# Performance work log

Measured on AMD Instinct MI355X. Metric: run time of the kernel, lower is better.

## Reference

```python
import jax, jax.numpy as jnp
import numpy as np

# Faithful distillation of AttentionNet's cross-modal attention block.
# The resnet50/PointNet backbones are replaced by their output feature maps
# (img: [B,256,64,64], pc2d: [B,2048,64,64]) supplied as inputs, since the
# kernel-relevant math is the conv1x1 projections + bmm/softmax/bmm attention,
# followed by global avg-pool, concat, and the fc + log_softmax head.
# Note: the original forward contains a bug (img_v1 overwritten by img.view)
# and dead code; we implement the clearly intended attention math.

B, CQ, CK, H, W = 16, 256, 2048, 64, 64
NUM_CLASS = 40


def conv1x1(x, w, b):
    # x: [B,Cin,H,W], w: [Cout,Cin], b: [Cout]
    return jnp.einsum('bchw,oc->bohw', x, w) + b[None, :, None, None]


def setup_inputs() -> dict:
    key = jax.random.key(0)
    ks = jax.random.split(key, 16)
    s = lambda fan_in: 1.0 / np.sqrt(fan_in)
    return {
        'img': jax.random.normal(ks[0], (B, CQ, H, W), jnp.float32),
        'pc2d': jax.random.normal(ks[1], (B, CK, H, W), jnp.float32),
        'Wq': jax.random.normal(ks[2], (CQ, CQ), jnp.float32) * s(CQ),
        'bq': jnp.zeros((CQ,), jnp.float32),
        'Wk': jax.random.normal(ks[3], (CQ, CK), jnp.float32) * s(CK),
        'bk': jnp.zeros((CQ,), jnp.float32),
        'Wvi': jax.random.normal(ks[4], (CQ, CQ), jnp.float32) * s(CQ),
        'bvi': jnp.zeros((CQ,), jnp.float32),
        'Wvp': jax.random.normal(ks[5], (CK, CK), jnp.float32) * s(CK),
        'bvp': jnp.zeros((CK,), jnp.float32),
        'gamma1': jnp.zeros((1,), jnp.float32),
        'W1': jax.random.normal(ks[6], (1024, CQ + CK), jnp.float32) * s(CQ + CK),
        'b1': jnp.zeros((1024,), jnp.float32),
        'W2': jax.random.normal(ks[7], (NUM_CLASS, 1024), jnp.float32) * s(1024),
        'b2': jnp.zeros((NUM_CLASS,), jnp.float32),
    }


def reference(img, pc2d, Wq, bq, Wk, bk, Wvi, bvi, Wvp, bvp, gamma1, W1, b1, W2, b2):
    N = H * W  # 4096
    q = conv1x1(img, Wq, bq).reshape(B, CQ, N).transpose(0, 2, 1)   # [B,N,256]
    k = conv1x1(pc2d, Wk, bk).reshape(B, CQ, N)                     # [B,256,N]
    att = jax.nn.softmax(jnp.einsum('bnc,bcm->bnm', q, k), axis=-1)  # [B,N,N]
    # image branch: out = gamma * bmm(V_img, att^T) + img
    vi = conv1x1(img, Wvi, bvi).reshape(B, CQ, N)
    img_att = jnp.einsum('bcn,bmn->bcm', vi, att).reshape(B, CQ, H, W)
    img_out = gamma1[0] * img_att + img
    # point-cloud branch: bmm(V_pc, att^T)
    vp = conv1x1(pc2d, Wvp, bvp).reshape(B, CK, N)
    pc_out = jnp.einsum('bcn,bmn->bcm', vp, att)                    # [B,2048,N]
    # global average pool + concat + MLP head with log_softmax
    img_feat = img_out.mean(axis=(2, 3))                            # [B,256]
    pc_feat = pc_out.mean(axis=2)                                   # [B,2048]
    fused = jnp.concatenate([img_feat, pc_feat], axis=-1)           # [B,2304]
    h = jax.nn.relu(fused @ W1.T + b1)
    logits = h @ W2.T + b2
    return jax.nn.log_softmax(logits, axis=1)
```

## Files before the change

### kernel.cpp

```cpp
#include <hip/hip_runtime.h>
#include <cstdint>

typedef __attribute__((ext_vector_type(8))) short short8;
typedef __attribute__((ext_vector_type(4))) float f32x4;

#define LOG2E 1.44269504088896340736f
#define SHIFT 64.0f

__device__ __forceinline__ unsigned short f2bf(float x) {
  union { float f; unsigned u; } c; c.f = x;
  unsigned r = c.u + 0x7fffu + ((c.u >> 16) & 1u);
  return (unsigned short)(r >> 16);
}

__device__ __forceinline__ void gl2lds16(const void* g, void* l) {
  __builtin_amdgcn_global_load_lds((const __attribute__((address_space(1))) void*)g,
                                   (__attribute__((address_space(3))) void*)l, 16, 0, 0);
}

__global__ void cvt_bf16(const float* __restrict__ src, unsigned short* __restrict__ dst, int n4) {
  int i = blockIdx.x * 256 + threadIdx.x;
  if (i >= n4) return;
  float4 v = ((const float4*)src)[i];
  ushort4 o;
  o.x = f2bf(v.x); o.y = f2bf(v.y); o.z = f2bf(v.z); o.w = f2bf(v.w);
  ((ushort4*)dst)[i] = o;
}

__device__ __forceinline__ void stage_resident(char* ldsbase, const char* src, int w, int lane) {
  const int p = lane & 31;
  const int rlo = lane >> 5;
#pragma unroll
  for (int it = 0; it < 16; ++it) {
    const int r = w * 32 + it * 2 + rlo;
    const int gs = (p & 24) | ((p & 7) ^ (r & 7));
    gl2lds16(src + (size_t)r * 512 + gs * 16, ldsbase + (w * 16 + it) * 1024);
  }
}

__device__ __forceinline__ void stage_stream(char* buf, const char* srcbase, int roff0, int roff1,
                                             int w) {
  gl2lds16(srcbase + roff0, buf + w * 1024);
  gl2lds16(srcbase + roff1, buf + 4096 + w * 1024);
}

__global__ __launch_bounds__(256, 2) void attn_rowsum(
    const unsigned short* __restrict__ qt, const unsigned short* __restrict__ kt,
    float* __restrict__ linv) {
  extern __shared__ char pool[];
  const int b = blockIdx.y, i0 = blockIdx.x * 128;
  const int t = threadIdx.x, w = t >> 6, lane = t & 63, q = lane >> 4, ln = lane & 15;
  const int ihalf = w >> 1, jhalf = w & 1;
  const char* qres = (const char*)(qt + ((size_t)b * 4096 + i0) * 256);
  const char* kb = (const char*)(kt + (size_t)b * 4096 * 256);
  const int rr0 = w * 16 + (lane >> 2);
  const int gsS = (lane & 3) ^ ((lane >> 3) & 3);
  const int roff0 = rr0 * 512 + gsS * 16;
  const int roff1 = (64 + rr0) * 512 + gsS * 16;
  const int aRow = (ihalf * 64 + ln) * 512;
  const int bRow = jhalf * 4096 + ln * 64 + (q ^ ((ln >> 1) & 3)) * 16;
  float lacc[4][4] = {};

  stage_resident(pool, qres, w, lane);
  stage_stream(pool + 65536, kb, roff0, roff1, w);
  __syncthreads();

  short8 ares[8][4];
#pragma unroll
  for (int c = 0; c < 8; ++c) {
    const int posA = ((4 * c) & 24) | ((4 * (c & 1) + q) ^ (ln & 7));
#pragma unroll
    for (int mt = 0; mt < 4; ++mt)
      ares[c][mt] = *(const short8*)(pool + aRow + mt * 8192 + posA * 16);
  }

#pragma unroll 1
  for (int jt = 0; jt < 32; ++jt) {
    f32x4 acc[4][4] = {};
#pragma unroll
    for (int c = 0; c < 8; ++c) {
      const int s = jt * 8 + c;
      if (s + 1 < 256) {
        const int njt = (s + 1) >> 3, nc = (s + 1) & 7;
        stage_stream(pool + 65536 + ((s + 1) & 1) * 8192,
                     kb + (size_t)njt * 65536 + nc * 64, roff0, roff1, w);
      }
      const char* B = pool + 65536 + (s & 1) * 8192;
      short8 bfr[4];
#pragma unroll
      for (int nt = 0; nt < 4; ++nt) bfr[nt] = *(const short8*)(B + bRow + nt * 1024);
#pragma unroll
      for (int mt = 0; mt < 4; ++mt)
#pragma unroll
        for (int nt = 0; nt < 4; ++nt)
          acc[mt][nt] =
              __builtin_amdgcn_mfma_f32_16x16x32_bf16(ares[c][mt], bfr[nt], acc[mt][nt], 0, 0, 0);
      __syncthreads();
    }
#pragma unroll
    for (int mt = 0; mt < 4; ++mt)
#pragma unroll
      for (int r = 0; r < 4; ++r) {
        float e = exp2f(acc[mt][0][r] * LOG2E - SHIFT) + exp2f(acc[mt][1][r] * LOG2E - SHIFT)
                + exp2f(acc[mt][2][r] * LOG2E - SHIFT) + exp2f(acc[mt][3][r] * LOG2E - SHIFT);
        e += __shfl_xor(e, 1); e += __shfl_xor(e, 2);
        e += __shfl_xor(e, 4); e += __shfl_xor(e, 8);
        lacc[mt][r] += e;
      }
  }
  float* lred = (float*)(pool + 65536);
  if (ln == 0) {
#pragma unroll
    for (int mt = 0; mt < 4; ++mt)
#pragma unroll
      for (int r = 0; r < 4; ++r)
        lred[jhalf * 128 + ihalf * 64 + mt * 16 + q * 4 + r] = lacc[mt][r];
  }
  __syncthreads();
  if (t < 128) linv[b * 4096 + i0 + t] = 1.0f / (lred[t] + lred[128 + t]);
}

__global__ __launch_bounds__(256, 2) void attn_colsum(
    const unsigned short* __restrict__ qt, const unsigned short* __restrict__ kt,
    const float* __restrict__ linv, float* __restrict__ s_col) {
  extern __shared__ char pool[];
  const int b = blockIdx.y, j0 = blockIdx.x * 128;
  const int t = threadIdx.x, w = t >> 6, lane = t & 63, q = lane >> 4, ln = lane & 15;
  const int ihalf = w >> 1, jhalf = w & 1;
  const char* kres = (const char*)(kt + ((size_t)b * 4096 + j0) * 256);
  const char* qb = (const char*)(qt + (size_t)b * 4096 * 256);
  const int rr0 = w * 16 + (lane >> 2);
  const int gsS = (lane & 3) ^ ((lane >> 3) & 3);
  const int roff0 = rr0 * 512 + gsS * 16;
  const int roff1 = (64 + rr0) * 512 + gsS * 16;
  const int aRow = ihalf * 4096 + ln * 64 + (q ^ ((ln >> 1) & 3)) * 16;
  const int bRow = (jhalf * 64 + ln) * 512;
  float scacc[4] = {};

  stage_resident(pool, kres, w, lane);
  stage_stream(pool + 65536, qb, roff0, roff1, w);
  __syncthreads();

  short8 bres[8][4];
#pragma unroll
  for (int c = 0; c < 8; ++c) {
    const int posB = ((4 * c) & 24) | ((4 * (c & 1) + q) ^ (ln & 7));
#pragma unroll
    for (int nt = 0; nt < 4; ++nt)
      bres[c][nt] = *(const short8*)(pool + bRow + nt * 8192 + posB * 16);
  }

#pragma unroll 1
  for (int it = 0; it < 32; ++it) {
    const float4* lp = (const float4*)(linv + (size_t)b * 4096 + it * 128 + ihalf * 64 + q * 4);
    float4 lv[4];
#pragma unroll
    for (int mt = 0; mt < 4; ++mt) lv[mt] = lp[mt * 4];

    f32x4 acc[4][4] = {};
#pragma unroll
    for (int c = 0; c < 8; ++c) {
      const int s = it * 8 + c;
      if (s + 1 < 256) {
        const int nit = (s + 1) >> 3, nc = (s + 1) & 7;
        stage_stream(pool + 65536 + ((s + 1) & 1) * 8192,
                     qb + (size_t)nit * 65536 + nc * 64, roff0, roff1, w);
      }
      const char* A = pool + 65536 + (s & 1) * 8192;
      short8 af[4];
#pragma unroll
      for (int mt = 0; mt < 4; ++mt) af[mt] = *(const short8*)(A + aRow + mt * 1024);
#pragma unroll
      for (int mt = 0; mt < 4; ++mt)
#pragma unroll
        for (int nt = 0; nt < 4; ++nt)
          acc[mt][nt] =
              __builtin_amdgcn_mfma_f32_16x16x32_bf16(af[mt], bres[c][nt], acc[mt][nt], 0, 0, 0);
      __syncthreads();
    }
#pragma unroll
    for (int nt = 0; nt < 4; ++nt) {
      float v = 0.f;
#pragma unroll
      for (int mt = 0; mt < 4; ++mt) {
        v += exp2f(acc[mt][nt][0] * LOG2E - SHIFT) * lv[mt].x;
        v += exp2f(acc[mt][nt][1] * LOG2E - SHIFT) * lv[mt].y;
        v += exp2f(acc[mt][nt][2] * LOG2E - SHIFT) * lv[mt].z;
        v += exp2f(acc[mt][nt][3] * LOG2E - SHIFT) * lv[mt].w;
      }
      v += __shfl_xor(v, 16); v += __shfl_xor(v, 32);
      scacc[nt] += v;
    }
  }
  float* sred = (float*)(pool + 65536);
  if (q == 0) {
#pragma unroll
    for (int nt = 0; nt < 4; ++nt)
      sred[ihalf * 128 + jhalf * 64 + nt * 16 + ln] = scacc[nt];
  }
  __syncthreads();
  if (t < 128) s_col[b * 4096 + j0 + t] = sred[t] + sred[128 + t];
}

__global__ __launch_bounds__(256, 2) void proj2_kernel(
    const float* __restrict__ In, const unsigned short* __restrict__ Wbf,
    const float* __restrict__ bias, unsigned short* __restrict__ Out, int Kdim) {
  __shared__ char Alds[128 * 144];
  __shared__ char Blds[256 * 128];
  const int b = blockIdx.y, sp0 = blockIdx.x * 128;
  const int t = threadIdx.x, w = t >> 6, lane = t & 63, q = lane >> 4, ln = lane & 15;
  const int shalf = w >> 1;
  const int cq = w & 1;
  const size_t wrow = (size_t)Kdim * 2;
  f32x4 acc[2][4][4] = {};
  const int nch = Kdim >> 6;

  const int brow0 = w * 8 + (lane >> 3);
  const int bgs = (lane & 7) ^ (lane >> 3);
  const int cp = t >> 3;
  const int spg = t & 7;

#pragma unroll 1
  for (int ch = 0; ch < nch; ++ch) {
    const int ci0 = ch * 64;
    const char* wsrc = (const char*)Wbf + (size_t)ci0 * 2 + bgs * 16;
#pragma unroll
    for (int i = 0; i < 8; ++i)
      gl2lds16(wsrc + (size_t)(brow0 + i * 32) * wrow, Blds + i * 4096 + w * 1024);
    {
      const float* r0 = In + ((size_t)b * Kdim + ci0 + 2 * cp) * 4096 + sp0 + spg * 16;
      const float* r1 = r0 + 4096;
#pragma unroll
      for (int h = 0; h < 2; ++h) {
        float4 a0 = *(const float4*)(r0 + h * 8);
        float4 a1 = *(const float4*)(r0 + h * 8 + 4);
        float4 b0 = *(const float4*)(r1 + h * 8);
        float4 b1 = *(const float4*)(r1 + h * 8 + 4);
        float va[8] = {a0.x, a0.y, a0.z, a0.w, a1.x, a1.y, a1.z, a1.w};
        float vb[8] = {b0.x, b0.y, b0.z, b0.w, b1.x, b1.y, b1.z, b1.w};
#pragma unroll
        for (int e = 0; e < 8; ++e) {
          const int spl = spg * 16 + h * 8 + e;
          const int colb = (cp << 2) ^ (((spl >> 4) & 7) << 4);
          unsigned u0 = f2bf(va[e]), u1 = f2bf(vb[e]);
          *(unsigned*)(Alds + spl * 144 + colb) = u0 | (u1 << 16);
        }
      }
    }
    __syncthreads();
#pragma unroll
    for (int ks = 0; ks < 2; ++ks) {
      short8 af[4], bfr[4];
#pragma unroll
      for (int mt = 0; mt < 4; ++mt) {
        const int row = shalf * 64 + mt * 16 + ln;
        const int colr = (ks * 64 + q * 16) ^ (((row >> 4) & 7) << 4);
        af[mt] = *(const short8*)(Alds + row * 144 + colr);
      }
#pragma unroll
      for (int cb = 0; cb < 2; ++cb) {
#pragma unroll
        for (int nt = 0; nt < 4; ++nt) {
          const int row = cb * 128 + cq * 64 + nt * 16 + ln;
          const int pos = (ks * 4 + q) ^ (ln & 7);
          bfr[nt] = *(const short8*)(Blds + row * 128 + pos * 16);
        }
#pragma unroll
        for (int mt = 0; mt < 4; ++mt)
#pragma unroll
          for (int nt = 0; nt < 4; ++nt)
            acc[cb][mt][nt] =
                __builtin_amdgcn_mfma_f32_16x16x32_bf16(af[mt], bfr[nt], acc[cb][mt][nt], 0, 0, 0);
      }
    }
    __syncthreads();
  }
#pragma unroll
  for (int cb = 0; cb < 2; ++cb)
#pragma unroll
    for (int nt = 0; nt < 4; ++nt) {
      const int co = cb * 128 + cq * 64 + nt * 16 + ln;
      const float bv = bias[co];
#pragma unroll
      for (int mt = 0; mt < 4; ++mt)
#pragma unroll
        for (int r = 0; r < 4; ++r) {
          const int sp = sp0 + shalf * 64 + mt * 16 + q * 4 + r;
          Out[((size_t)b * 4096 + sp) * 256 + co] = f2bf(acc[cb][mt][nt][r] + bv);
        }
    }
}

__global__ void sbar_kernel(const float* __restrict__ s_col, float* __restrict__ sbar) {
  const int b = blockIdx.x, t = threadIdx.x;
  float v = 0.f;
  for (int k = 0; k < 16; ++k) v += s_col[b * 4096 + t + 256 * k];
  for (int m = 1; m < 64; m <<= 1) v += __shfl_xor(v, m);
  __shared__ float red[4];
  if ((t & 63) == 0) red[t >> 6] = v;
  __syncthreads();
  if (t == 0) sbar[b] = (red[0] + red[1] + red[2] + red[3]) * (1.f / 4096.f);
}

__global__ __launch_bounds__(256) void pool2_kernel(
    const float* __restrict__ img, const float* __restrict__ pc2d,
    const float* __restrict__ s_col, float* __restrict__ u_pool,
    float* __restrict__ imean, float* __restrict__ t_pool) {
  const int t = threadIdx.x, w = t >> 6, lane = t & 63;
  const int gid = blockIdx.x * 4 + w;
  const int b = gid / 2304, c = gid - b * 2304;
  const bool isimg = c < 256;
  const float4* row4 = isimg
      ? (const float4*)(img + ((size_t)b * 256 + c) * 4096)
      : (const float4*)(pc2d + ((size_t)b * 2048 + (c - 256)) * 4096);
  const float4* s4 = (const float4*)(s_col + (size_t)b * 4096);
  float accd = 0.f, accs = 0.f;
#pragma unroll
  for (int kk = 0; kk < 16; ++kk) {
    float4 x = row4[lane + 64 * kk];
    float4 sv = s4[lane + 64 * kk];
    accd += x.x * sv.x + x.y * sv.y + x.z * sv.z + x.w * sv.w;
    accs += x.x + x.y + x.z + x.w;
  }
#pragma unroll
  for (int m = 1; m < 64; m <<= 1) {
    accd += __shfl_xor(accd, m);
    accs += __shfl_xor(accs, m);
  }
  if (lane == 0) {
    if (isimg) {
      u_pool[b * 256 + c] = accd * (1.f / 4096.f);
      imean[b * 256 + c] = accs * (1.f / 4096.f);
    } else {
      t_pool[b * 2048 + (c - 256)] = accd * (1.f / 4096.f);
    }
  }
}

__global__ void imgfeat_kernel(const float* __restrict__ Wvi, const float* __restrict__ bvi,
                               const float* __restrict__ gamma1, const float* __restrict__ u_pool,
                               const float* __restrict__ imean, const float* __restrict__ sbar,
                               float* __restrict__ fused) {
  const int t = threadIdx.x;
  const int co = blockIdx.x * 64 + (t >> 2), j = t & 3;
  float acc[16];
#pragma unroll
  for (int b = 0; b < 16; ++b) acc[b] = 0.f;
  const float4* w4 = (const float4*)(Wvi + (size_t)co * 256);
  for (int kk = 0; kk < 16; ++kk) {
    float4 wv = w4[j + 4 * kk];
#pragma unroll
    for (int b = 0; b < 16; ++b) {
      float4 uv = ((const float4*)(u_pool + b * 256))[j + 4 * kk];
      acc[b] += wv.x * uv.x + wv.y * uv.y + wv.z * uv.z + wv.w * uv.w;
    }
  }
#pragma unroll
  for (int b = 0; b < 16; ++b) { acc[b] += __shfl_xor(acc[b], 1); acc[b] += __shfl_xor(acc[b], 2); }
  if (j == 0) {
    float g = gamma1[0], bv = bvi[co];
#pragma unroll
    for (int b = 0; b < 16; ++b)
      fused[b * 2304 + co] = g * (acc[b] + bv * sbar[b]) + imean[b * 256 + co];
  }
}

__global__ void pcfeat_kernel(const float* __restrict__ Wvp, const float* __restrict__ bvp,
                              const float* __restrict__ t_pool, const float* __restrict__ sbar,
                              float* __restrict__ fused) {
  const int t = threadIdx.x;
  const int co = blockIdx.x * 64 + (t >> 2), j = t & 3;
  float acc[16];
#pragma unroll
  for (int b = 0; b < 16; ++b) acc[b] = 0.f;
  const float4* w4 = (const float4*)(Wvp + (size_t)co * 2048);
  for (int kk = 0; kk < 128; ++kk) {
    float4 wv = w4[j + 4 * kk];
#pragma unroll
    for (int b = 0; b < 16; ++b) {
      float4 tv = ((const float4*)(t_pool + b * 2048))[j + 4 * kk];
      acc[b] += wv.x * tv.x + wv.y * tv.y + wv.z * tv.z + wv.w * tv.w;
    }
  }
#pragma unroll
  for (int b = 0; b < 16; ++b) { acc[b] += __shfl_xor(acc[b], 1); acc[b] += __shfl_xor(acc[b], 2); }
  if (j == 0) {
    float bv = bvp[co];
#pragma unroll
    for (int b = 0; b < 16; ++b)
      fused[b * 2304 + 256 + co] = acc[b] + bv * sbar[b];
  }
}

__global__ void head1_kernel(const float* __restrict__ W1, const float* __restrict__ b1,
                             const float* __restrict__ fused, float* __restrict__ h) {
  const int t = threadIdx.x;
  const int o = blockIdx.x * 64 + (t >> 2), j = t & 3;
  float acc[16];
#pragma unroll
  for (int b = 0; b < 16; ++b) acc[b] = 0.f;
  const float4* w4 = (const float4*)(W1 + (size_t)o * 2304);
  for (int kk = 0; kk < 144; ++kk) {
    float4 wv = w4[j + 4 * kk];
#pragma unroll
    for (int b = 0; b < 16; ++b) {
      float4 fv = ((const float4*)(fused + b * 2304))[j + 4 * kk];
      acc[b] += wv.x * fv.x + wv.y * fv.y + wv.z * fv.z + wv.w * fv.w;
    }
  }
#pragma unroll
  for (int b = 0; b < 16; ++b) { acc[b] += __shfl_xor(acc[b], 1); acc[b] += __shfl_xor(acc[b], 2); }
  if (j == 0) {
    float bv = b1[o];
#pragma unroll
    for (int b = 0; b < 16; ++b) h[b * 1024 + o] = fmaxf(acc[b] + bv, 0.f);
  }
}

__global__ void head2_kernel(const float* __restrict__ W2, const float* __restrict__ b2,
                             const float* __restrict__ h, float* __restrict__ out) {
  const int b = blockIdx.x, t = threadIdx.x;
  __shared__ float logit[40];
  __shared__ float red[4];
  float4 hv = ((const float4*)(h + b * 1024))[t];
  for (int c = 0; c < 40; ++c) {
    float4 wv = ((const float4*)(W2 + (size_t)c * 1024))[t];
    float p = wv.x * hv.x + wv.y * hv.y + wv.z * hv.z + wv.w * hv.w;
    for (int m = 1; m < 64; m <<= 1) p += __shfl_xor(p, m);
    if ((t & 63) == 0) red[t >> 6] = p;
    __syncthreads();
    if (t == 0) logit[c] = red[0] + red[1] + red[2] + red[3] + b2[c];
    __syncthreads();
  }
  if (t == 0) {
    float mx = -1e30f;
    for (int c = 0; c < 40; ++c) mx = fmaxf(mx, logit[c]);
    float s = 0.f;
    for (int c = 0; c < 40; ++c) s += expf(logit[c] - mx);
    float ls = logf(s);
    for (int c = 0; c < 40; ++c) out[b * 40 + c] = logit[c] - mx - ls;
  }
}

extern "C" void kernel_launch(void* const* d_in, const int* in_sizes, int n_in,
                              void* d_out, int out_size, void* d_ws, size_t ws_size,
                              hipStream_t stream) {
  (void)in_sizes; (void)n_in; (void)out_size; (void)ws_size;
  const float* img    = (const float*)d_in[0];
  const float* pc2d   = (const float*)d_in[1];
  const float* Wq     = (const float*)d_in[2];
  const float* bq     = (const float*)d_in[3];
  const float* Wk     = (const float*)d_in[4];
  const float* bk     = (const float*)d_in[5];
  const float* Wvi    = (const float*)d_in[6];
  const float* bvi    = (const float*)d_in[7];
  const float* Wvp    = (const float*)d_in[8];
  const float* bvp    = (const float*)d_in[9];
  const float* gamma1 = (const float*)d_in[10];
  const float* W1     = (const float*)d_in[11];
  const float* b1     = (const float*)d_in[12];
  const float* W2     = (const float*)d_in[13];
  const float* b2     = (const float*)d_in[14];

  char* ws = (char*)d_ws;
  unsigned short* q_t   = (unsigned short*)(ws + 0);
  unsigned short* k_t   = (unsigned short*)(ws + 33554432);
  unsigned short* wq_bf = (unsigned short*)(ws + 67108864);
  unsigned short* wk_bf = (unsigned short*)(ws + 67239936);
  float* linv   = (float*)(ws + 68288512);
  float* s_col  = (float*)(ws + 68812800);
  float* sbar   = (float*)(ws + 69074944);
  float* u_pool = (float*)(ws + 69075008);
  float* imean  = (float*)(ws + 69091392);
  float* t_pool = (float*)(ws + 69107776);
  float* fusedb = (float*)(ws + 69238848);
  float* h_buf  = (float*)(ws + 69386304);

  hipFuncSetAttribute((const void*)attn_rowsum, hipFuncAttributeMaxDynamicSharedMemorySize, 81920);
  hipFuncSetAttribute((const void*)attn_colsum, hipFuncAttributeMaxDynamicSharedMemorySize, 81920);

  cvt_bf16<<<dim3(64), dim3(256), 0, stream>>>(Wq, wq_bf, 16384);
  cvt_bf16<<<dim3(512), dim3(256), 0, stream>>>(Wk, wk_bf, 131072);

  proj2_kernel<<<dim3(32, 16), dim3(256), 0, stream>>>(img, wq_bf, bq, q_t, 256);
  proj2_kernel<<<dim3(32, 16), dim3(256), 0, stream>>>(pc2d, wk_bf, bk, k_t, 2048);

  attn_rowsum<<<dim3(32, 16), dim3(256), 81920, stream>>>(q_t, k_t, linv);
  attn_colsum<<<dim3(32, 16), dim3(256), 81920, stream>>>(q_t, k_t, linv, s_col);

  sbar_kernel<<<dim3(16), dim3(256), 0, stream>>>(s_col, sbar);
  pool2_kernel<<<dim3(9216), dim3(256), 0, stream>>>(img, pc2d, s_col, u_pool, imean, t_pool);

  imgfeat_kernel<<<dim3(4), dim3(256), 0, stream>>>(Wvi, bvi, gamma1, u_pool, imean, sbar, fusedb);
  pcfeat_kernel<<<dim3(32), dim3(256), 0, stream>>>(Wvp, bvp, t_pool, sbar, fusedb);

  head1_kernel<<<dim3(16), dim3(256), 0, stream>>>(W1, b1, fusedb, h_buf);
  head2_kernel<<<dim3(16), dim3(256), 0, stream>>>(W2, b2, h_buf, (float*)d_out);
}
```

Measured before the change: 1.593 ms.

## Deepen K/Q stream prefetch to a 4-slot ring and halve resident LDS staging

The attention row/column-sum kernels now stage the resident Q (or K) tile in two 32KB halves. Each half is loaded into registers by the waves that own it, shrinking dynamic LDS from 80KB to 64KB. The streamed operand uses a 4-slot ring with a prefetch distance of three steps instead of a double buffer one step ahead, to better hide global-to-LDS latency. In the row-sum kernel, the B fragment reads from LDS are also issued one step ahead into a second register buffer. The split staging adds extra barriers at kernel start, and the register double-buffering increases register pressure.

Result: slower. 1.682 ms (+5.6%).

```diff
diff --git a/kernel.cpp b/kernel.cpp
--- a/kernel.cpp
+++ b/kernel.cpp
@@ -27,14 +27,14 @@
   ((ushort4*)dst)[i] = o;
 }
 
-__device__ __forceinline__ void stage_resident(char* ldsbase, const char* src, int w, int lane) {
+__device__ __forceinline__ void stage_resident_half(char* lds, const char* src, int w, int lane) {
   const int p = lane & 31;
   const int rlo = lane >> 5;
 #pragma unroll
-  for (int it = 0; it < 16; ++it) {
-    const int r = w * 32 + it * 2 + rlo;
-    const int gs = (p & 24) | ((p & 7) ^ (r & 7));
-    gl2lds16(src + (size_t)r * 512 + gs * 16, ldsbase + (w * 16 + it) * 1024);
+  for (int it = 0; it < 8; ++it) {
+    const int rl = w * 16 + it * 2 + rlo;
+    const int gs = (p & 24) | ((p & 7) ^ (rl & 7));
+    gl2lds16(src + (size_t)rl * 512 + gs * 16, lds + (w * 8 + it) * 1024);
   }
 }
 
@@ -57,21 +57,38 @@
   const int gsS = (lane & 3) ^ ((lane >> 3) & 3);
   const int roff0 = rr0 * 512 + gsS * 16;
   const int roff1 = (64 + rr0) * 512 + gsS * 16;
-  const int aRow = (ihalf * 64 + ln) * 512;
   const int bRow = jhalf * 4096 + ln * 64 + (q ^ ((ln >> 1) & 3)) * 16;
+  char* sbuf = pool + 32768;
   float lacc[4][4] = {};
-
-  stage_resident(pool, qres, w, lane);
-  stage_stream(pool + 65536, kb, roff0, roff1, w);
-  __syncthreads();
-
-  short8 ares[8][4];
-#pragma unroll
-  for (int c = 0; c < 8; ++c) {
-    const int posA = ((4 * c) & 24) | ((4 * (c & 1) + q) ^ (ln & 7));
-#pragma unroll
-    for (int mt = 0; mt < 4; ++mt)
-      ares[c][mt] = *(const short8*)(pool + aRow + mt * 8192 + posA * 16);
+  short8 ares[8][4], bfr[2][4];
+
+  stage_resident_half(pool, qres, w, lane);
+  stage_stream(sbuf, kb, roff0, roff1, w);
+  stage_stream(sbuf + 8192, kb + 64, roff0, roff1, w);
+  stage_stream(sbuf + 16384, kb + 128, roff0, roff1, w);
+  __syncthreads();
+  if (ihalf == 0) {
+#pragma unroll
+    for (int c = 0; c < 8; ++c) {
+      const int posA = ((4 * c) & 24) | ((4 * (c & 1) + q) ^ (ln & 7));
+#pragma unroll
+      for (int mt = 0; mt < 4; ++mt)
+        ares[c][mt] = *(const short8*)(pool + (mt * 16 + ln) * 512 + posA * 16);
+    }
+  }
+#pragma unroll
+  for (int nt = 0; nt < 4; ++nt) bfr[0][nt] = *(const short8*)(sbuf + bRow + nt * 1024);
+  __syncthreads();
+  stage_resident_half(pool, qres + 64 * 512, w, lane);
+  __syncthreads();
+  if (ihalf == 1) {
+#pragma unroll
+    for (int c = 0; c < 8; ++c) {
+      const int posA = ((4 * c) & 24) | ((4 * (c & 1) + q) ^ (ln & 7));
+#pragma unroll
+      for (int mt = 0; mt < 4; ++mt)
+        ares[c][mt] = *(const short8*)(pool + (mt * 16 + ln) * 512 + posA * 16);
+    }
   }
 
 #pragma unroll 1
@@ -80,21 +97,23 @@
 #pragma unroll
     for (int c = 0; c < 8; ++c) {
       const int s = jt * 8 + c;
-      if (s + 1 < 256) {
-        const int njt = (s + 1) >> 3, nc = (s + 1) & 7;
-        stage_stream(pool + 65536 + ((s + 1) & 1) * 8192,
-                     kb + (size_t)njt * 65536 + nc * 64, roff0, roff1, w);
-      }
-      const char* B = pool + 65536 + (s & 1) * 8192;
-      short8 bfr[4];
-#pragma unroll
-      for (int nt = 0; nt < 4; ++nt) bfr[nt] = *(const short8*)(B + bRow + nt * 1024);
+      if (s < 253) {
+        const int m = s + 3;
+        stage_stream(sbuf + (m & 3) * 8192, kb + (size_t)(m >> 3) * 65536 + (m & 7) * 64,
+                     roff0, roff1, w);
+      }
+      if (s < 255) {
+        const char* Bn = sbuf + ((s + 1) & 3) * 8192;
+#pragma unroll
+        for (int nt = 0; nt < 4; ++nt)
+          bfr[(c + 1) & 1][nt] = *(const short8*)(Bn + bRow + nt * 1024);
+      }
 #pragma unroll
       for (int mt = 0; mt < 4; ++mt)
 #pragma unroll
         for (int nt = 0; nt < 4; ++nt)
-          acc[mt][nt] =
-              __builtin_amdgcn_mfma_f32_16x16x32_bf16(ares[c][mt], bfr[nt], acc[mt][nt], 0, 0, 0);
+          acc[mt][nt] = __builtin_amdgcn_mfma_f32_16x16x32_bf16(ares[c][mt], bfr[c & 1][nt],
+                                                                acc[mt][nt], 0, 0, 0);
       __syncthreads();
     }
 #pragma unroll
@@ -108,7 +127,7 @@
         lacc[mt][r] += e;
       }
   }
-  float* lred = (float*)(pool + 65536);
+  float* lred = (float*)pool;
   if (ln == 0) {
 #pragma unroll
     for (int mt = 0; mt < 4; ++mt)
@@ -134,20 +153,35 @@
   const int roff0 = rr0 * 512 + gsS * 16;
   const int roff1 = (64 + rr0) * 512 + gsS * 16;
   const int aRow = ihalf * 4096 + ln * 64 + (q ^ ((ln >> 1) & 3)) * 16;
-  const int bRow = (jhalf * 64 + ln) * 512;
+  char* sbuf = pool + 32768;
   float scacc[4] = {};
-
-  stage_resident(pool, kres, w, lane);
-  stage_stream(pool + 65536, qb, roff0, roff1, w);
-  __syncthreads();
-
   short8 bres[8][4];
-#pragma unroll
-  for (int c = 0; c < 8; ++c) {
-    const int posB = ((4 * c) & 24) | ((4 * (c & 1) + q) ^ (ln & 7));
-#pragma unroll
-    for (int nt = 0; nt < 4; ++nt)
-      bres[c][nt] = *(const short8*)(pool + bRow + nt * 8192 + posB * 16);
+
+  stage_resident_half(pool, kres, w, lane);
+  stage_stream(sbuf, qb, roff0, roff1, w);
+  stage_stream(sbuf + 8192, qb + 64, roff0, roff1, w);
+  stage_stream(sbuf + 16384, qb + 128, roff0, roff1, w);
+  __syncthreads();
+  if (jhalf == 0) {
+#pragma unroll
+    for (int c = 0; c < 8; ++c) {
+      const int posB = ((4 * c) & 24) | ((4 * (c & 1) + q) ^ (ln & 7));
+#pragma unroll
+      for (int nt = 0; nt < 4; ++nt)
+        bres[c][nt] = *(const short8*)(pool + (nt * 16 + ln) * 512 + posB * 16);
+    }
+  }
+  __syncthreads();
+  stage_resident_half(pool, kres + 64 * 512, w, lane);
+  __syncthreads();
+  if (jhalf == 1) {
+#pragma unroll
+    for (int c = 0; c < 8; ++c) {
+      const int posB = ((4 * c) & 24) | ((4 * (c & 1) + q) ^ (ln & 7));
+#pragma unroll
+      for (int nt = 0; nt < 4; ++nt)
+        bres[c][nt] = *(const short8*)(pool + (nt * 16 + ln) * 512 + posB * 16);
+    }
   }
 
 #pragma unroll 1
@@ -161,12 +195,12 @@
 #pragma unroll
     for (int c = 0; c < 8; ++c) {
       const int s = it * 8 + c;
-      if (s + 1 < 256) {
-        const int nit = (s + 1) >> 3, nc = (s + 1) & 7;
-        stage_stream(pool + 65536 + ((s + 1) & 1) * 8192,
-                     qb + (size_t)nit * 65536 + nc * 64, roff0, roff1, w);
-      }
-      const char* A = pool + 65536 + (s & 1) * 8192;
+      if (s < 253) {
+        const int m = s + 3;
+        stage_stream(sbuf + (m & 3) * 8192, qb + (size_t)(m >> 3) * 65536 + (m & 7) * 64,
+                     roff0, roff1, w);
+      }
+      const char* A = sbuf + (s & 3) * 8192;
       short8 af[4];
 #pragma unroll
       for (int mt = 0; mt < 4; ++mt) af[mt] = *(const short8*)(A + aRow + mt * 1024);
@@ -192,7 +226,7 @@
       scacc[nt] += v;
     }
   }
-  float* sred = (float*)(pool + 65536);
+  float* sred = (float*)pool;
   if (q == 0) {
 #pragma unroll
     for (int nt = 0; nt < 4; ++nt)
@@ -476,8 +510,8 @@
   float* fusedb = (float*)(ws + 69238848);
   float* h_buf  = (float*)(ws + 69386304);
 
-  hipFuncSetAttribute((const void*)attn_rowsum, hipFuncAttributeMaxDynamicSharedMemorySize, 81920);
-  hipFuncSetAttribute((const void*)attn_colsum, hipFuncAttributeMaxDynamicSharedMemorySize, 81920);
+  hipFuncSetAttribute((const void*)attn_rowsum, hipFuncAttributeMaxDynamicSharedMemorySize, 65536);
+  hipFuncSetAttribute((const void*)attn_colsum, hipFuncAttributeMaxDynamicSharedMemorySize, 65536);
 
   cvt_bf16<<<dim3(64), dim3(256), 0, stream>>>(Wq, wq_bf, 16384);
   cvt_bf16<<<dim3(512), dim3(256), 0, stream>>>(Wk, wk_bf, 131072);
@@ -485,8 +519,8 @@
   proj2_kernel<<<dim3(32, 16), dim3(256), 0, stream>>>(img, wq_bf, bq, q_t, 256);
   proj2_kernel<<<dim3(32, 16), dim3(256), 0, stream>>>(pc2d, wk_bf, bk, k_t, 2048);
 
-  attn_rowsum<<<dim3(32, 16), dim3(256), 81920, stream>>>(q_t, k_t, linv);
-  attn_colsum<<<dim3(32, 16), dim3(256), 81920, stream>>>(q_t, k_t, linv, s_col);
+  attn_rowsum<<<dim3(32, 16), dim3(256), 65536, stream>>>(q_t, k_t, linv);
+  attn_colsum<<<dim3(32, 16), dim3(256), 65536, stream>>>(q_t, k_t, linv, s_col);
 
   sbar_kernel<<<dim3(16), dim3(256), 0, stream>>>(s_col, sbar);
   pool2_kernel<<<dim3(9216), dim3(256), 0, stream>>>(img, pc2d, s_col, u_pool, imean, t_pool);
```
